# Performance work log

Measured on AMD Instinct MI355X. Metric: run time of the kernel, lower is better.

Reference implementation:

```python
import jax, jax.numpy as jnp
import numpy as np

DIM = 1024
HEADS = 8
HEAD_DIM = DIM // HEADS
FFN = 4096
B, N = 32, 1024
EPS = 1e-5


def layer_norm(x, g, b):
    mu = jnp.mean(x, axis=-1, keepdims=True)
    var = jnp.mean(jnp.square(x - mu), axis=-1, keepdims=True)
    return (x - mu) * jax.lax.rsqrt(var + EPS) * g + b


def setup_inputs() -> dict:
    key = jax.random.key(0)
    ks = jax.random.split(key, 10)
    s = 0.02
    return {
        "x": jax.random.normal(ks[0], (B, N, DIM), dtype=jnp.float32),
        "haltingscore": jnp.zeros((B, N), dtype=jnp.float32),
        "Wq": jax.random.normal(ks[1], (DIM, DIM), dtype=jnp.float32) * s,
        "Wkv": jax.random.normal(ks[2], (DIM, 2 * DIM), dtype=jnp.float32) * s,
        "Wp": jax.random.normal(ks[3], (DIM, DIM), dtype=jnp.float32) * s,
        "bp": jnp.zeros((DIM,), dtype=jnp.float32),
        "W1": jax.random.normal(ks[4], (DIM, FFN), dtype=jnp.float32) * s,
        "b1": jnp.zeros((FFN,), dtype=jnp.float32),
        "W2": jax.random.normal(ks[5], (FFN, DIM), dtype=jnp.float32) * s,
        "b2": jnp.zeros((DIM,), dtype=jnp.float32),
        "ln1_g": jnp.ones((DIM,), dtype=jnp.float32),
        "ln1_b": jnp.zeros((DIM,), dtype=jnp.float32),
        "ln2_g": jnp.ones((DIM,), dtype=jnp.float32),
        "ln2_b": jnp.zeros((DIM,), dtype=jnp.float32),
    }


def reference(x, haltingscore, Wq, Wkv, Wp, bp, W1, b1, W2, b2,
              ln1_g, ln1_b, ln2_g, ln2_b):
    b, n, c = x.shape
    scale = HEAD_DIM ** -0.5
    # ---- EfficientAttention (explicit QK^T softmax V) ----
    q = (x @ Wq).reshape(b, n, HEADS, HEAD_DIM).transpose(0, 2, 1, 3)  # bhnd
    kv = (x @ Wkv).reshape(b, n, 2, HEADS, HEAD_DIM).transpose(2, 0, 3, 1, 4)
    k, v = kv[0], kv[1]                                               # bhnd
    attn = jax.nn.softmax(jnp.einsum('bhnd,bhmd->bhnm', q, k) * scale, axis=-1)
    o = jnp.einsum('bhnm,bhmd->bhnd', attn, v)
    o = o.transpose(0, 2, 1, 3).reshape(b, n, c)
    o = o @ Wp + bp
    attn_mean = jnp.mean(attn, axis=1)                                # (B, N, N)
    # ---- residual + LN1 ----
    h = layer_norm(x + o, ln1_g, ln1_b)
    # ---- FFN + residual + LN2 ----
    ff = jax.nn.relu(h @ W1 + b1) @ W2 + b2
    out = layer_norm(h + ff, ln2_g, ln2_b)
    # ---- halting score update ----
    a = jax.nn.softmax(jnp.sum(attn_mean, axis=1), axis=-1)           # (B, N)
    halting = haltingscore + a
    return (out, halting, a)
```

## Files before the change

### kernel.cpp

```cpp
#include <hip/hip_runtime.h>
#include <hip/hip_bf16.h>
#include <stdint.h>

#define DIMC 1024
#define HEADS 8
#define HDIM 128
#define FFND 4096
#define BATCH 32
#define SEQ 1024
#define SROWS (BATCH*SEQ)
#define QSTR 3072

typedef unsigned short u16;
typedef short short4v __attribute__((ext_vector_type(4)));
typedef short short8 __attribute__((ext_vector_type(8)));
typedef float f32x4 __attribute__((ext_vector_type(4)));
typedef __bf16 bf16x8 __attribute__((ext_vector_type(8)));

__device__ __forceinline__ u16 f2bf(float f) {
    union { float f; uint32_t u; } x{f};
    uint32_t r = x.u + 0x7FFFu + ((x.u >> 16) & 1u);
    return (u16)(r >> 16);
}
__device__ __forceinline__ float bf2f(u16 h) {
    union { uint32_t u; float f; } x;
    x.u = ((uint32_t)h) << 16;
    return x.f;
}

__device__ __forceinline__ f32x4 mfma16(short8 a, short8 b, f32x4 c) {
    return __builtin_amdgcn_mfma_f32_16x16x32_bf16(
        __builtin_bit_cast(bf16x8, a), __builtin_bit_cast(bf16x8, b), c, 0, 0, 0);
}

__device__ __forceinline__ void gload_lds16(const u16* g, u16* lds) {
    __builtin_amdgcn_global_load_lds(
        (const __attribute__((address_space(1))) uint32_t*)g,
        (__attribute__((address_space(3))) uint32_t*)lds, 16, 0, 0);
}

__global__ __launch_bounds__(256) void k_cast(const float* __restrict__ in,
                                              u16* __restrict__ out, int n4) {
    int i = blockIdx.x * 256 + threadIdx.x;
    if (i < n4) {
        f32x4 v = ((const f32x4*)in)[i];
        uint32_t lo = f2bf(v[0]) | ((uint32_t)f2bf(v[1]) << 16);
        uint32_t hi = f2bf(v[2]) | ((uint32_t)f2bf(v[3]) << 16);
        ((uint2*)out)[i] = make_uint2(lo, hi);
    }
}

__global__ __launch_bounds__(256) void k_transpose_cast(const float* __restrict__ W,
                                                        u16* __restrict__ Wt,
                                                        int K, int N) {
    __shared__ u16 tile[32][33];
    int n0 = blockIdx.x * 32, k0 = blockIdx.y * 32;
    int tx = threadIdx.x, ty = threadIdx.y;
#pragma unroll
    for (int i = 0; i < 32; i += 8)
        tile[ty + i][tx] = f2bf(W[(size_t)(k0 + ty + i) * N + n0 + tx]);
    __syncthreads();
#pragma unroll
    for (int i = 0; i < 32; i += 8)
        Wt[(size_t)(n0 + ty + i) * K + k0 + tx] = tile[tx][ty + i];
}

template<bool OUT_BF16, bool RELU, bool BIAS, bool VSPLIT>
__global__ __launch_bounds__(512, 2) void k_gemm256(const u16* __restrict__ A,
                                                    const u16* __restrict__ Bt,
                                                    const float* __restrict__ bias,
                                                    void* __restrict__ C,
                                                    u16* __restrict__ Vt,
                                                    int M, int N, int K) {
    union Smem {
        struct { u16 A[4][8192]; u16 B[4][8192]; } k;
        u16 ob[64 * 264];
        float of[64 * 268];
        u16 vt[256 * 66];
    };
    __shared__ Smem smem;
    const int tid = threadIdx.x;
    const int lane = tid & 63, wv = tid >> 6;
    const int wm = wv >> 2, wn = wv & 3;
    const int l15 = lane & 15, lg = lane >> 4;
    const int gx = gridDim.x;
    const int nwg = gx * gridDim.y;
    const int id = blockIdx.y * gx + blockIdx.x;
    const int id2 = (id & 7) * (nwg >> 3) + (id >> 3);
    const int row0 = (id2 / gx) << 8, col0 = (id2 % gx) << 8;
    const int NT = K >> 5;

#define STAGE_A(tt) {                                                          \
    int _t = (tt);                                                             \
    _Pragma("unroll")                                                          \
    for (int i = 0; i < 2; ++i) {                                              \
        int blk = wv * 2 + i;                                                  \
        gload_lds16(A + (size_t)(row0 + blk * 16 + l15) * K + _t * 32 + lg * 8,\
                    &smem.k.A[_t & 3][blk * 512]);                             \
    } }
#define STAGE_B(tt) {                                                          \
    int _t = (tt);                                                             \
    _Pragma("unroll")                                                          \
    for (int i = 0; i < 2; ++i) {                                              \
        int blk = wv * 2 + i;                                                  \
        gload_lds16(Bt + (size_t)(col0 + blk * 16 + l15) * K + _t * 32 + lg * 8,\
                    &smem.k.B[_t & 3][blk * 512]);                             \
    } }

    STAGE_A(0); STAGE_B(0);
    STAGE_A(1); STAGE_B(1);
    STAGE_A(2); STAGE_B(2);

    f32x4 acc[8][4] = {};
    for (int t = 0; t < NT; ++t) {
        const int slot = t & 3;
        if (t <= NT - 3)      asm volatile("s_waitcnt vmcnt(8)" ::: "memory");
        else if (t == NT - 2) asm volatile("s_waitcnt vmcnt(4)" ::: "memory");
        else                  asm volatile("s_waitcnt vmcnt(0)" ::: "memory");
        __builtin_amdgcn_s_barrier();
        __builtin_amdgcn_sched_barrier(0);

        const u16* Ab = &smem.k.A[slot][(wm * 8) * 512];
        const u16* Bb = &smem.k.B[slot][(wn * 4) * 512];

        if (t + 3 < NT) STAGE_A(t + 3);
        short8 bf[4], af[4];
#pragma unroll
        for (int n = 0; n < 4; ++n) bf[n] = *(const short8*)(Bb + n * 512 + lane * 8);
#pragma unroll
        for (int m = 0; m < 4; ++m) af[m] = *(const short8*)(Ab + m * 512 + lane * 8);
        __builtin_amdgcn_s_setprio(1);
#pragma unroll
        for (int m = 0; m < 4; ++m)
#pragma unroll
            for (int n = 0; n < 4; ++n)
                acc[m][n] = mfma16(af[m], bf[n], acc[m][n]);
        __builtin_amdgcn_s_setprio(0);

        if (t + 3 < NT) STAGE_B(t + 3);
#pragma unroll
        for (int m = 0; m < 4; ++m) af[m] = *(const short8*)(Ab + (4 + m) * 512 + lane * 8);
        __builtin_amdgcn_s_setprio(1);
#pragma unroll
        for (int m = 0; m < 4; ++m)
#pragma unroll
            for (int n = 0; n < 4; ++n)
                acc[4 + m][n] = mfma16(af[m], bf[n], acc[4 + m][n]);
        __builtin_amdgcn_s_setprio(0);
    }
#undef STAGE_A
#undef STAGE_B

    const bool vpath = VSPLIT && (col0 >= 2048);
    __syncthreads();
#pragma unroll
    for (int s = 0; s < 4; ++s) {
        if (s) __syncthreads();
        if (wm == (s >> 1)) {
            const int mb4 = (s & 1) * 4;
#pragma unroll
            for (int mm = 0; mm < 4; ++mm)
#pragma unroll
                for (int n = 0; n < 4; ++n) {
                    int c = wn * 64 + n * 16 + l15;
                    float bv = BIAS ? bias[col0 + c] : 0.f;
#pragma unroll
                    for (int j = 0; j < 4; ++j) {
                        int lr = mm * 16 + lg * 4 + j;
                        float v = acc[mb4 + mm][n][j] + bv;
                        if (RELU) v = fmaxf(v, 0.f);
                        if (vpath)         smem.vt[c * 66 + lr] = f2bf(v);
                        else if (OUT_BF16) smem.ob[lr * 264 + c] = f2bf(v);
                        else               smem.of[lr * 268 + c] = v;
                    }
                }
        }
        __syncthreads();
        const int gr0 = row0 + s * 64;
        if (vpath) {
            const int bb = gr0 >> 10;
            const int mb = gr0 & 1023;
#pragma unroll
            for (int it = 0; it < 4; ++it) {
                int idx = it * 512 + tid;
                int dc = idx >> 3, mseg = idx & 7;
                int hh = (col0 - 2048 + dc) >> 7;
                int dd = (col0 - 2048 + dc) & 127;
                *(short8*)(Vt + ((size_t)(bb * 8 + hh)) * (HDIM * SEQ)
                              + (size_t)dd * SEQ + mb + mseg * 8) =
                    *(const short8*)(&smem.vt[dc * 66 + mseg * 8]);
            }
        } else if (OUT_BF16) {
#pragma unroll
            for (int it = 0; it < 4; ++it) {
                int idx = it * 512 + tid;
                int r = idx >> 5, seg = idx & 31;
                *(short8*)((u16*)C + (size_t)(gr0 + r) * N + col0 + seg * 8) =
                    *(const short8*)(&smem.ob[r * 264 + seg * 8]);
            }
        } else {
#pragma unroll
            for (int it = 0; it < 8; ++it) {
                int idx = it * 512 + tid;
                int r = idx >> 6, seg = idx & 63;
                *(f32x4*)((float*)C + (size_t)(gr0 + r) * N + col0 + seg * 4) =
                    *(const f32x4*)(&smem.of[r * 268 + seg * 4]);
            }
        }
    }
}

__global__ __launch_bounds__(512, 6) void k_attn(const u16* __restrict__ QKV,
                                                 const u16* __restrict__ Vt,
                                                 u16* __restrict__ O,
                                                 float* __restrict__ csp) {
    __shared__ u16 Kl[2][4096];
    __shared__ u16 Vl[2][4096];
    __shared__ u16 p_lds[8][640];
    __shared__ float cs[1024];
    const int id = blockIdx.x;
    const int id2 = (id & 7) * 256 + (id >> 3);
    const int qt = id2 & 7, bh = id2 >> 3;
    const int b = bh >> 3, h = bh & 7;
    const int tid = threadIdx.x, lane = tid & 63, wv = tid >> 6;
    const int l15 = lane & 15, lg = lane >> 4;

    for (int i = tid; i < 1024; i += 512) cs[i] = 0.f;

    const int q0 = qt * 128 + wv * 16;
    const u16* qbase = QKV + (size_t)(b * SEQ + q0 + l15) * QSTR + h * HDIM + lg * 8;
    short8 qf[4];
#pragma unroll
    for (int kk = 0; kk < 4; ++kk) qf[kk] = *(const short8*)(qbase + kk * 32);
    const float CEXP = 0.12751743f;
    const u16* kbase = QKV + (size_t)(b * SEQ) * QSTR + 1024 + h * HDIM;
    const u16* vtb = Vt + (size_t)bh * HDIM * SEQ;

    const int sg = wv >> 2, skk = wv & 3;

#define STAGE_K(tt) gload_lds16(kbase + (size_t)((tt) * 32 + sg * 16 + l15) * QSTR \
                                + skk * 32 + lg * 8, &Kl[(tt) & 1][wv * 512]);
#define STAGE_V(tt) gload_lds16(vtb + (size_t)(wv * 16 + l15) * SEQ + (tt) * 32    \
                                + lg * 8, &Vl[(tt) & 1][wv * 512]);

    STAGE_K(0);
    asm volatile("s_waitcnt vmcnt(0)" ::: "memory");
    __builtin_amdgcn_s_barrier();
    f32x4 rs = {0.f, 0.f, 0.f, 0.f};
    for (int t = 0; t < 32; ++t) {
        if (t < 31) STAGE_K(t + 1);
        const u16* Kp = &Kl[t & 1][0];
        f32x4 s0 = {0.f, 0.f, 0.f, 0.f}, s1 = {0.f, 0.f, 0.f, 0.f};
        __builtin_amdgcn_s_setprio(1);
#pragma unroll
        for (int kk = 0; kk < 4; ++kk) {
            short8 b0 = *(const short8*)(Kp + kk * 512 + lane * 8);
            short8 b1 = *(const short8*)(Kp + (4 + kk) * 512 + lane * 8);
            s0 = mfma16(qf[kk], b0, s0);
            s1 = mfma16(qf[kk], b1, s1);
        }
        __builtin_amdgcn_s_setprio(0);
#pragma unroll
        for (int r = 0; r < 4; ++r)
            rs[r] += __builtin_amdgcn_exp2f(s0[r] * CEXP)
                   + __builtin_amdgcn_exp2f(s1[r] * CEXP);
        asm volatile("s_waitcnt vmcnt(0)" ::: "memory");
        __builtin_amdgcn_s_barrier();
    }
#pragma unroll
    for (int o = 1; o < 16; o <<= 1)
#pragma unroll
        for (int r = 0; r < 4; ++r) rs[r] += __shfl_xor(rs[r], o);
    f32x4 inv_rs;
#pragma unroll
    for (int r = 0; r < 4; ++r) inv_rs[r] = 1.f / rs[r];

    STAGE_K(0); STAGE_V(0);
    asm volatile("s_waitcnt vmcnt(0)" ::: "memory");
    __builtin_amdgcn_s_barrier();
    f32x4 od[8] = {};
    u16* pl = &p_lds[wv][0];
    for (int t = 0; t < 32; ++t) {
        const int m0 = t * 32;
        if (t < 31) { STAGE_K(t + 1); STAGE_V(t + 1); }
        const u16* Kp = &Kl[t & 1][0];
        f32x4 s0 = {0.f, 0.f, 0.f, 0.f}, s1 = {0.f, 0.f, 0.f, 0.f};
        __builtin_amdgcn_s_setprio(1);
#pragma unroll
        for (int kk = 0; kk < 4; ++kk) {
            short8 b0 = *(const short8*)(Kp + kk * 512 + lane * 8);
            short8 b1 = *(const short8*)(Kp + (4 + kk) * 512 + lane * 8);
            s0 = mfma16(qf[kk], b0, s0);
            s1 = mfma16(qf[kk], b1, s1);
        }
        __builtin_amdgcn_s_setprio(0);
        float p0[4], p1[4];
#pragma unroll
        for (int r = 0; r < 4; ++r) {
            p0[r] = __builtin_amdgcn_exp2f(s0[r] * CEXP) * inv_rs[r];
            p1[r] = __builtin_amdgcn_exp2f(s1[r] * CEXP) * inv_rs[r];
        }
        float c0 = p0[0] + p0[1] + p0[2] + p0[3];
        float c1 = p1[0] + p1[1] + p1[2] + p1[3];
        c0 += __shfl_xor(c0, 16); c0 += __shfl_xor(c0, 32);
        c1 += __shfl_xor(c1, 16); c1 += __shfl_xor(c1, 32);
        if (lane < 16)      atomicAdd(&cs[m0 + lane], c0);
        else if (lane < 32) atomicAdd(&cs[m0 + lane], c1);
#pragma unroll
        for (int r = 0; r < 4; ++r) {
            pl[(lg * 4 + r) * 40 + l15]      = f2bf(p0[r]);
            pl[(lg * 4 + r) * 40 + 16 + l15] = f2bf(p1[r]);
        }
        short8 pa = *(const short8*)(pl + l15 * 40 + lg * 8);
        const u16* Vb_ = &Vl[t & 1][0];
        __builtin_amdgcn_s_setprio(1);
#pragma unroll
        for (int db = 0; db < 8; ++db) {
            short8 vf = *(const short8*)(Vb_ + db * 512 + lane * 8);
            od[db] = mfma16(pa, vf, od[db]);
        }
        __builtin_amdgcn_s_setprio(0);
        asm volatile("s_waitcnt vmcnt(0)" ::: "memory");
        __builtin_amdgcn_s_barrier();
    }
#undef STAGE_K
#undef STAGE_V
    __syncthreads();
    u16* ob = O + (size_t)(b * SEQ + q0 + lg * 4) * DIMC + h * HDIM + l15;
#pragma unroll
    for (int db = 0; db < 8; ++db)
#pragma unroll
        for (int r = 0; r < 4; ++r)
            ob[(size_t)r * DIMC + db * 16] = f2bf(od[db][r]);
    for (int m = tid; m < 1024; m += 512)
        csp[((size_t)bh * 8 + qt) * 1024 + m] = cs[m];
}

__global__ __launch_bounds__(256) void k_ln1(const float* __restrict__ xa,
                                             const u16* __restrict__ pj,
                                             const float* __restrict__ g,
                                             const float* __restrict__ bt,
                                             u16* __restrict__ ob) {
    const int row = blockIdx.x;
    const int t = threadIdx.x, lane = t & 63, wv = t >> 6;
    f32x4 va = ((const f32x4*)(xa + (size_t)row * DIMC))[t];
    short4v hv = ((const short4v*)(pj + (size_t)row * DIMC))[t];
    f32x4 s;
#pragma unroll
    for (int j = 0; j < 4; ++j) s[j] = va[j] + bf2f((u16)hv[j]);
    float sum = s[0] + s[1] + s[2] + s[3];
    float sq = s[0]*s[0] + s[1]*s[1] + s[2]*s[2] + s[3]*s[3];
#pragma unroll
    for (int o = 1; o < 64; o <<= 1) { sum += __shfl_xor(sum, o); sq += __shfl_xor(sq, o); }
    __shared__ float red[8];
    if (lane == 0) { red[wv] = sum; red[4 + wv] = sq; }
    __syncthreads();
    sum = red[0] + red[1] + red[2] + red[3];
    sq  = red[4] + red[5] + red[6] + red[7];
    float mu = sum * (1.f / DIMC);
    float rstd = rsqrtf(sq * (1.f / DIMC) - mu * mu + 1e-5f);
    f32x4 gg = ((const f32x4*)g)[t];
    f32x4 bb = ((const f32x4*)bt)[t];
    uint32_t lo, hi;
    float o0 = (s[0] - mu) * rstd * gg[0] + bb[0];
    float o1 = (s[1] - mu) * rstd * gg[1] + bb[1];
    float o2 = (s[2] - mu) * rstd * gg[2] + bb[2];
    float o3 = (s[3] - mu) * rstd * gg[3] + bb[3];
    lo = f2bf(o0) | ((uint32_t)f2bf(o1) << 16);
    hi = f2bf(o2) | ((uint32_t)f2bf(o3) << 16);
    ((uint2*)(ob + (size_t)row * DIMC))[t] = make_uint2(lo, hi);
}

__global__ __launch_bounds__(256) void k_ln2(const u16* __restrict__ xa,
                                             const u16* __restrict__ f2,
                                             const float* __restrict__ g,
                                             const float* __restrict__ bt,
                                             float* __restrict__ of) {
    const int row = blockIdx.x;
    const int t = threadIdx.x, lane = t & 63, wv = t >> 6;
    short4v hv = ((const short4v*)(xa + (size_t)row * DIMC))[t];
    short4v fv = ((const short4v*)(f2 + (size_t)row * DIMC))[t];
    f32x4 s;
#pragma unroll
    for (int j = 0; j < 4; ++j) s[j] = bf2f((u16)hv[j]) + bf2f((u16)fv[j]);
    float sum = s[0] + s[1] + s[2] + s[3];
    float sq = s[0]*s[0] + s[1]*s[1] + s[2]*s[2] + s[3]*s[3];
#pragma unroll
    for (int o = 1; o < 64; o <<= 1) { sum += __shfl_xor(sum, o); sq += __shfl_xor(sq, o); }
    __shared__ float red[8];
    if (lane == 0) { red[wv] = sum; red[4 + wv] = sq; }
    __syncthreads();
    sum = red[0] + red[1] + red[2] + red[3];
    sq  = red[4] + red[5] + red[6] + red[7];
    float mu = sum * (1.f / DIMC);
    float rstd = rsqrtf(sq * (1.f / DIMC) - mu * mu + 1e-5f);
    f32x4 gg = ((const f32x4*)g)[t];
    f32x4 bb = ((const f32x4*)bt)[t];
    f32x4 o4;
#pragma unroll
    for (int j = 0; j < 4; ++j) o4[j] = (s[j] - mu) * rstd * gg[j] + bb[j];
    ((f32x4*)(of + (size_t)row * DIMC))[t] = o4;
}

__global__ __launch_bounds__(256) void k_halt(const float* __restrict__ csp,
                                              const float* __restrict__ hs,
                                              float* __restrict__ halt_out,
                                              float* __restrict__ a_out) {
    const int b = blockIdx.x, t = threadIdx.x, lane = t & 63, wv = t >> 6;
    const float* base = csp + (size_t)b * 65536;
    float acc[4] = {0.f, 0.f, 0.f, 0.f};
    for (int s2 = 0; s2 < 64; ++s2) {
#pragma unroll
        for (int j = 0; j < 4; ++j) acc[j] += base[(size_t)s2 * 1024 + j * 256 + t];
    }
    float mx = -1e30f;
#pragma unroll
    for (int j = 0; j < 4; ++j) { acc[j] *= 0.125f; mx = fmaxf(mx, acc[j]); }
#pragma unroll
    for (int o = 1; o < 64; o <<= 1) mx = fmaxf(mx, __shfl_xor(mx, o));
    __shared__ float red[8];
    if (lane == 0) red[wv] = mx;
    __syncthreads();
    mx = fmaxf(fmaxf(red[0], red[1]), fmaxf(red[2], red[3]));
    float e[4]; float sum = 0.f;
#pragma unroll
    for (int j = 0; j < 4; ++j) { e[j] = __expf(acc[j] - mx); sum += e[j]; }
#pragma unroll
    for (int o = 1; o < 64; o <<= 1) sum += __shfl_xor(sum, o);
    if (lane == 0) red[4 + wv] = sum;
    __syncthreads();
    sum = red[4] + red[5] + red[6] + red[7];
    float inv = 1.f / sum;
#pragma unroll
    for (int j = 0; j < 4; ++j) {
        int m = j * 256 + t;
        float a = e[j] * inv;
        a_out[b * SEQ + m] = a;
        halt_out[b * SEQ + m] = hs[b * SEQ + m] + a;
    }
}

extern "C" void kernel_launch(void* const* d_in, const int* in_sizes, int n_in,
                              void* d_out, int out_size, void* d_ws, size_t ws_size,
                              hipStream_t stream) {
    (void)in_sizes; (void)n_in; (void)out_size; (void)ws_size;
    const float* x   = (const float*)d_in[0];
    const float* hs  = (const float*)d_in[1];
    const float* Wq  = (const float*)d_in[2];
    const float* Wkv = (const float*)d_in[3];
    const float* Wp  = (const float*)d_in[4];
    const float* bp  = (const float*)d_in[5];
    const float* W1  = (const float*)d_in[6];
    const float* b1  = (const float*)d_in[7];
    const float* W2  = (const float*)d_in[8];
    const float* b2  = (const float*)d_in[9];
    const float* g1  = (const float*)d_in[10];
    const float* be1 = (const float*)d_in[11];
    const float* g2  = (const float*)d_in[12];
    const float* be2 = (const float*)d_in[13];

    float* out = (float*)d_out;
    float* halt_out = out + (size_t)SROWS * DIMC;
    float* a_out = halt_out + SROWS;

    char* w = (char*)d_ws;
    const size_t MB = 1024 * 1024;
    u16*  xb    = (u16*)(w);
    u16*  qkv   = (u16*)(w + 64 * MB);
    u16*  Vt    = (u16*)(w + 256 * MB);
    u16*  WqkvT = (u16*)(w + 320 * MB);
    u16*  WpT   = (u16*)(w + 326 * MB);
    u16*  W1T   = (u16*)(w + 328 * MB);
    u16*  W2T   = (u16*)(w + 336 * MB);
    float* csp  = (float*)(w + 344 * MB);
    u16*  o_b   = (u16*)(w);
    u16*  projb = (u16*)(w + 64 * MB);
    u16*  hb    = (u16*)(w);
    u16*  ff1   = (u16*)(w + 64 * MB);
    u16*  ff2b  = (u16*)(w + 192 * MB);

    dim3 tb(32, 8);
    k_cast<<<SROWS * DIMC / 4 / 256, 256, 0, stream>>>(x, xb, SROWS * DIMC / 4);
    k_transpose_cast<<<dim3(DIMC / 32, DIMC / 32), tb, 0, stream>>>(Wq, WqkvT, DIMC, DIMC);
    k_transpose_cast<<<dim3(2 * DIMC / 32, DIMC / 32), tb, 0, stream>>>(
        Wkv, WqkvT + (size_t)DIMC * DIMC, DIMC, 2 * DIMC);
    k_transpose_cast<<<dim3(DIMC / 32, DIMC / 32), tb, 0, stream>>>(Wp, WpT, DIMC, DIMC);
    k_transpose_cast<<<dim3(FFND / 32, DIMC / 32), tb, 0, stream>>>(W1, W1T, DIMC, FFND);
    k_transpose_cast<<<dim3(DIMC / 32, FFND / 32), tb, 0, stream>>>(W2, W2T, FFND, DIMC);
    k_gemm256<true, false, false, true><<<dim3(QSTR / 256, SROWS / 256), 512, 0, stream>>>(
        xb, WqkvT, nullptr, qkv, Vt, SROWS, QSTR, DIMC);
    k_attn<<<2048, 512, 0, stream>>>(qkv, Vt, o_b, csp);
    k_gemm256<true, false, true, false><<<dim3(DIMC / 256, SROWS / 256), 512, 0, stream>>>(
        o_b, WpT, bp, projb, nullptr, SROWS, DIMC, DIMC);
    k_ln1<<<SROWS, 256, 0, stream>>>(x, projb, g1, be1, hb);
    for (int c = 0; c < 2; ++c) {
        const size_t ro = (size_t)c * 16384;
        k_gemm256<true, true, true, false><<<dim3(FFND / 256, 16384 / 256), 512, 0, stream>>>(
            hb + ro * DIMC, W1T, b1, ff1, nullptr, 16384, FFND, DIMC);
        k_gemm256<true, false, true, false><<<dim3(DIMC / 256, 16384 / 256), 512, 0, stream>>>(
            ff1, W2T, b2, ff2b, nullptr, 16384, DIMC, FFND);
        k_ln2<<<16384, 256, 0, stream>>>(hb + ro * DIMC, ff2b, g2, be2, out + ro * DIMC);
    }
    k_halt<<<BATCH, 256, 0, stream>>>(csp, hs, halt_out, a_out);
}
```

Measured before the change: 1.519 ms.

## Process two 16-row query tiles per wave in attention kernel with 256 threads

The attention kernel now runs 4 waves per block instead of 8, and each wave handles 32 query rows as two 16-row tiles sharing the same K and V fragments read from LDS. Each wave issues twice as many staging loads so the block still fills the K/V tiles. The aim is to halve LDS reads of K/V per MFMA and cut barrier participants. The cost is more VGPRs for two sets of accumulators and less latency hiding from fewer waves.

```diff
diff --git a/kernel.cpp b/kernel.cpp
--- a/kernel.cpp
+++ b/kernel.cpp
@@ -210,13 +210,13 @@
     }
 }
 
-__global__ __launch_bounds__(512, 6) void k_attn(const u16* __restrict__ QKV,
+__global__ __launch_bounds__(256, 3) void k_attn(const u16* __restrict__ QKV,
                                                  const u16* __restrict__ Vt,
                                                  u16* __restrict__ O,
                                                  float* __restrict__ csp) {
     __shared__ u16 Kl[2][4096];
     __shared__ u16 Vl[2][4096];
-    __shared__ u16 p_lds[8][640];
+    __shared__ u16 p_lds[4][1280];
     __shared__ float cs[1024];
     const int id = blockIdx.x;
     const int id2 = (id & 7) * 256 + (id >> 3);
@@ -225,99 +225,128 @@
     const int tid = threadIdx.x, lane = tid & 63, wv = tid >> 6;
     const int l15 = lane & 15, lg = lane >> 4;
 
-    for (int i = tid; i < 1024; i += 512) cs[i] = 0.f;
-
-    const int q0 = qt * 128 + wv * 16;
-    const u16* qbase = QKV + (size_t)(b * SEQ + q0 + l15) * QSTR + h * HDIM + lg * 8;
-    short8 qf[4];
-#pragma unroll
-    for (int kk = 0; kk < 4; ++kk) qf[kk] = *(const short8*)(qbase + kk * 32);
+    for (int i = tid; i < 1024; i += 256) cs[i] = 0.f;
+
+    const int q0 = qt * 128 + wv * 32;
+    const u16* qbaseA = QKV + (size_t)(b * SEQ + q0 + l15) * QSTR + h * HDIM + lg * 8;
+    const u16* qbaseB = qbaseA + (size_t)16 * QSTR;
+    short8 qfA[4], qfB[4];
+#pragma unroll
+    for (int kk = 0; kk < 4; ++kk) {
+        qfA[kk] = *(const short8*)(qbaseA + kk * 32);
+        qfB[kk] = *(const short8*)(qbaseB + kk * 32);
+    }
     const float CEXP = 0.12751743f;
     const u16* kbase = QKV + (size_t)(b * SEQ) * QSTR + 1024 + h * HDIM;
     const u16* vtb = Vt + (size_t)bh * HDIM * SEQ;
 
-    const int sg = wv >> 2, skk = wv & 3;
-
-#define STAGE_K(tt) gload_lds16(kbase + (size_t)((tt) * 32 + sg * 16 + l15) * QSTR \
-                                + skk * 32 + lg * 8, &Kl[(tt) & 1][wv * 512]);
-#define STAGE_V(tt) gload_lds16(vtb + (size_t)(wv * 16 + l15) * SEQ + (tt) * 32    \
-                                + lg * 8, &Vl[(tt) & 1][wv * 512]);
+#define STAGE_K(tt) { _Pragma("unroll")                                         \
+    for (int i = 0; i < 2; ++i) { int c = wv * 2 + i;                           \
+        gload_lds16(kbase + (size_t)((tt) * 32 + (c >> 2) * 16 + l15) * QSTR    \
+                    + (c & 3) * 32 + lg * 8, &Kl[(tt) & 1][c * 512]); } }
+#define STAGE_V(tt) { _Pragma("unroll")                                         \
+    for (int i = 0; i < 2; ++i) { int c = wv * 2 + i;                           \
+        gload_lds16(vtb + (size_t)(c * 16 + l15) * SEQ + (tt) * 32 + lg * 8,    \
+                    &Vl[(tt) & 1][c * 512]); } }
 
     STAGE_K(0);
     asm volatile("s_waitcnt vmcnt(0)" ::: "memory");
     __builtin_amdgcn_s_barrier();
-    f32x4 rs = {0.f, 0.f, 0.f, 0.f};
+    f32x4 rsA = {0.f, 0.f, 0.f, 0.f}, rsB = {0.f, 0.f, 0.f, 0.f};
     for (int t = 0; t < 32; ++t) {
         if (t < 31) STAGE_K(t + 1);
         const u16* Kp = &Kl[t & 1][0];
-        f32x4 s0 = {0.f, 0.f, 0.f, 0.f}, s1 = {0.f, 0.f, 0.f, 0.f};
+        f32x4 sA0 = {0.f,0.f,0.f,0.f}, sA1 = {0.f,0.f,0.f,0.f};
+        f32x4 sB0 = {0.f,0.f,0.f,0.f}, sB1 = {0.f,0.f,0.f,0.f};
         __builtin_amdgcn_s_setprio(1);
 #pragma unroll
         for (int kk = 0; kk < 4; ++kk) {
             short8 b0 = *(const short8*)(Kp + kk * 512 + lane * 8);
             short8 b1 = *(const short8*)(Kp + (4 + kk) * 512 + lane * 8);
-            s0 = mfma16(qf[kk], b0, s0);
-            s1 = mfma16(qf[kk], b1, s1);
+            sA0 = mfma16(qfA[kk], b0, sA0);
+            sA1 = mfma16(qfA[kk], b1, sA1);
+            sB0 = mfma16(qfB[kk], b0, sB0);
+            sB1 = mfma16(qfB[kk], b1, sB1);
         }
         __builtin_amdgcn_s_setprio(0);
 #pragma unroll
-        for (int r = 0; r < 4; ++r)
-            rs[r] += __builtin_amdgcn_exp2f(s0[r] * CEXP)
-                   + __builtin_amdgcn_exp2f(s1[r] * CEXP);
+        for (int r = 0; r < 4; ++r) {
+            rsA[r] += __builtin_amdgcn_exp2f(sA0[r] * CEXP)
+                    + __builtin_amdgcn_exp2f(sA1[r] * CEXP);
+            rsB[r] += __builtin_amdgcn_exp2f(sB0[r] * CEXP)
+                    + __builtin_amdgcn_exp2f(sB1[r] * CEXP);
+        }
         asm volatile("s_waitcnt vmcnt(0)" ::: "memory");
         __builtin_amdgcn_s_barrier();
     }
 #pragma unroll
     for (int o = 1; o < 16; o <<= 1)
 #pragma unroll
-        for (int r = 0; r < 4; ++r) rs[r] += __shfl_xor(rs[r], o);
-    f32x4 inv_rs;
-#pragma unroll
-    for (int r = 0; r < 4; ++r) inv_rs[r] = 1.f / rs[r];
+        for (int r = 0; r < 4; ++r) {
+            rsA[r] += __shfl_xor(rsA[r], o);
+            rsB[r] += __shfl_xor(rsB[r], o);
+        }
+    f32x4 inv_rsA, inv_rsB;
+#pragma unroll
+    for (int r = 0; r < 4; ++r) {
+        inv_rsA[r] = 1.f / rsA[r];
+        inv_rsB[r] = 1.f / rsB[r];
+    }
 
     STAGE_K(0); STAGE_V(0);
     asm volatile("s_waitcnt vmcnt(0)" ::: "memory");
     __builtin_amdgcn_s_barrier();
-    f32x4 od[8] = {};
+    f32x4 odA[8] = {}, odB[8] = {};
     u16* pl = &p_lds[wv][0];
     for (int t = 0; t < 32; ++t) {
         const int m0 = t * 32;
         if (t < 31) { STAGE_K(t + 1); STAGE_V(t + 1); }
         const u16* Kp = &Kl[t & 1][0];
-        f32x4 s0 = {0.f, 0.f, 0.f, 0.f}, s1 = {0.f, 0.f, 0.f, 0.f};
+        f32x4 sA0 = {0.f,0.f,0.f,0.f}, sA1 = {0.f,0.f,0.f,0.f};
+        f32x4 sB0 = {0.f,0.f,0.f,0.f}, sB1 = {0.f,0.f,0.f,0.f};
         __builtin_amdgcn_s_setprio(1);
 #pragma unroll
         for (int kk = 0; kk < 4; ++kk) {
             short8 b0 = *(const short8*)(Kp + kk * 512 + lane * 8);
             short8 b1 = *(const short8*)(Kp + (4 + kk) * 512 + lane * 8);
-            s0 = mfma16(qf[kk], b0, s0);
-            s1 = mfma16(qf[kk], b1, s1);
+            sA0 = mfma16(qfA[kk], b0, sA0);
+            sA1 = mfma16(qfA[kk], b1, sA1);
+            sB0 = mfma16(qfB[kk], b0, sB0);
+            sB1 = mfma16(qfB[kk], b1, sB1);
         }
         __builtin_amdgcn_s_setprio(0);
-        float p0[4], p1[4];
+        float pA0[4], pA1[4], pB0[4], pB1[4];
 #pragma unroll
         for (int r = 0; r < 4; ++r) {
-            p0[r] = __builtin_amdgcn_exp2f(s0[r] * CEXP) * inv_rs[r];
-            p1[r] = __builtin_amdgcn_exp2f(s1[r] * CEXP) * inv_rs[r];
-        }
-        float c0 = p0[0] + p0[1] + p0[2] + p0[3];
-        float c1 = p1[0] + p1[1] + p1[2] + p1[3];
+            pA0[r] = __builtin_amdgcn_exp2f(sA0[r] * CEXP) * inv_rsA[r];
+            pA1[r] = __builtin_amdgcn_exp2f(sA1[r] * CEXP) * inv_rsA[r];
+            pB0[r] = __builtin_amdgcn_exp2f(sB0[r] * CEXP) * inv_rsB[r];
+            pB1[r] = __builtin_amdgcn_exp2f(sB1[r] * CEXP) * inv_rsB[r];
+        }
+        float c0 = pA0[0] + pA0[1] + pA0[2] + pA0[3]
+                 + pB0[0] + pB0[1] + pB0[2] + pB0[3];
+        float c1 = pA1[0] + pA1[1] + pA1[2] + pA1[3]
+                 + pB1[0] + pB1[1] + pB1[2] + pB1[3];
         c0 += __shfl_xor(c0, 16); c0 += __shfl_xor(c0, 32);
         c1 += __shfl_xor(c1, 16); c1 += __shfl_xor(c1, 32);
         if (lane < 16)      atomicAdd(&cs[m0 + lane], c0);
         else if (lane < 32) atomicAdd(&cs[m0 + lane], c1);
 #pragma unroll
         for (int r = 0; r < 4; ++r) {
-            pl[(lg * 4 + r) * 40 + l15]      = f2bf(p0[r]);
-            pl[(lg * 4 + r) * 40 + 16 + l15] = f2bf(p1[r]);
-        }
-        short8 pa = *(const short8*)(pl + l15 * 40 + lg * 8);
+            pl[(lg * 4 + r) * 40 + l15]           = f2bf(pA0[r]);
+            pl[(lg * 4 + r) * 40 + 16 + l15]      = f2bf(pA1[r]);
+            pl[(16 + lg * 4 + r) * 40 + l15]      = f2bf(pB0[r]);
+            pl[(16 + lg * 4 + r) * 40 + 16 + l15] = f2bf(pB1[r]);
+        }
+        short8 paA = *(const short8*)(pl + l15 * 40 + lg * 8);
+        short8 paB = *(const short8*)(pl + (16 + l15) * 40 + lg * 8);
         const u16* Vb_ = &Vl[t & 1][0];
         __builtin_amdgcn_s_setprio(1);
 #pragma unroll
         for (int db = 0; db < 8; ++db) {
             short8 vf = *(const short8*)(Vb_ + db * 512 + lane * 8);
-            od[db] = mfma16(pa, vf, od[db]);
+            odA[db] = mfma16(paA, vf, odA[db]);
+            odB[db] = mfma16(paB, vf, odB[db]);
         }
         __builtin_amdgcn_s_setprio(0);
         asm volatile("s_waitcnt vmcnt(0)" ::: "memory");
@@ -326,13 +355,16 @@
 #undef STAGE_K
 #undef STAGE_V
     __syncthreads();
-    u16* ob = O + (size_t)(b * SEQ + q0 + lg * 4) * DIMC + h * HDIM + l15;
+    u16* obA = O + (size_t)(b * SEQ + q0 + lg * 4) * DIMC + h * HDIM + l15;
+    u16* obB = obA + (size_t)16 * DIMC;
 #pragma unroll
     for (int db = 0; db < 8; ++db)
 #pragma unroll
-        for (int r = 0; r < 4; ++r)
-            ob[(size_t)r * DIMC + db * 16] = f2bf(od[db][r]);
-    for (int m = tid; m < 1024; m += 512)
+        for (int r = 0; r < 4; ++r) {
+            obA[(size_t)r * DIMC + db * 16] = f2bf(odA[db][r]);
+            obB[(size_t)r * DIMC + db * 16] = f2bf(odB[db][r]);
+        }
+    for (int m = tid; m < 1024; m += 256)
         csp[((size_t)bh * 8 + qt) * 1024 + m] = cs[m];
 }
 
@@ -489,7 +521,7 @@
     k_transpose_cast<<<dim3(DIMC / 32, FFND / 32), tb, 0, stream>>>(W2, W2T, FFND, DIMC);
     k_gemm256<true, false, false, true><<<dim3(QSTR / 256, SROWS / 256), 512, 0, stream>>>(
         xb, WqkvT, nullptr, qkv, Vt, SROWS, QSTR, DIMC);
-    k_attn<<<2048, 512, 0, stream>>>(qkv, Vt, o_b, csp);
+    k_attn<<<2048, 256, 0, stream>>>(qkv, Vt, o_b, csp);
     k_gemm256<true, false, true, false><<<dim3(DIMC / 256, SROWS / 256), 512, 0, stream>>>(
         o_b, WpT, bp, projb, nullptr, SROWS, DIMC, DIMC);
     k_ln1<<<SROWS, 256, 0, stream>>>(x, projb, g1, be1, hb);
```

Result: faster. 1.472 ms (-3.1%).
